# Performance work log

Measured on AMD Instinct MI355X. Metric: run time of the kernel, lower is better.

The kernel has to match this reference:

```python
import jax, jax.numpy as jnp
import numpy as np

N_NODES = 100000
N_EDGES = 1600000
D_IN = 128
D_OUT = 128


def setup_inputs() -> dict:
    key = jax.random.key(0)
    k1, k2, k3, k4 = jax.random.split(key, 4)
    feat = jax.random.normal(k1, (N_NODES, D_IN), dtype=jnp.float32)
    weight = jax.random.normal(k2, (D_IN, D_OUT), dtype=jnp.float32) * (1.0 / np.sqrt(D_IN))
    src = jax.random.randint(k3, (N_EDGES,), 0, N_NODES, dtype=jnp.int64)
    dst = jax.random.randint(k4, (N_EDGES,), 0, N_NODES, dtype=jnp.int64)
    return {"feat": feat, "weight": weight, "src": src, "dst": dst}


def reference(feat, weight, src, dst):
    n = feat.shape[0]
    ones = jnp.ones(src.shape[0], dtype=feat.dtype)
    # norm == 'both': scale source features by out_degree^{-1/2}
    out_deg = jnp.clip(jax.ops.segment_sum(ones, src, num_segments=n), 1.0)
    feat_src = feat * (out_deg ** -0.5)[:, None]  # [N, D_in]
    # update_all(copy_src, sum): gather src features, segment-sum into dst
    agg = jax.ops.segment_sum(feat_src[src], dst, num_segments=n)  # [N, D_in]
    # dense transform with external weight
    rst = agg @ weight  # [N, D_out]
    # destination-side normalization by in_degree^{-1/2}
    in_deg = jnp.clip(jax.ops.segment_sum(ones, dst, num_segments=n), 1.0)
    rst = rst * (in_deg ** -0.5)[:, None]
    return rst
```

## Files before the change

### kernel.cpp

```cpp
#include <hip/hip_runtime.h>
#include <stdint.h>


#define DIM 128
#define BK 64
#define MAXB 2048
#define CAPB 1280
#define SK 128
#define MAXS 1024
#define CAPS 2560
#define PT 512
#define EPT 13
#define CHUNK (PT * EPT)

typedef unsigned int uint;
typedef unsigned short ushortT;
typedef __attribute__((ext_vector_type(8))) _Float16 f16x8;
typedef __attribute__((ext_vector_type(4))) float f32x4;

__device__ __forceinline__ ushortT f2bf(float x) {
    uint u = __float_as_uint(x);
    u = (u + 0x7FFFu + ((u >> 16) & 1u)) >> 16;
    return (ushortT)u;
}
__device__ __forceinline__ float bflo(uint u) { return __uint_as_float(u << 16); }
__device__ __forceinline__ float bfhi(uint u) { return __uint_as_float(u & 0xffff0000u); }

union H16 { _Float16 h; ushortT u; };
__device__ __forceinline__ ushortT f2h_bits(float x) {
    H16 t; t.h = (_Float16)x; return t.u;
}

#define OFF_CD    0
#define OFF_LOFD  8192
#define OFF_CS    16384
#define OFF_LOFS  20480
#define OFF_BUFD  24576
#define OFF_BUFB  51200
#define OFF_BUFS  64512
#define OFF_WTOT  71168
#define SMEM_SZ   71232

__global__ __launch_bounds__(PT) void fusedA(
    const int* __restrict__ src, const int* __restrict__ dst,
    int* __restrict__ curB, int* __restrict__ curS,
    int* __restrict__ pairs, unsigned char* __restrict__ srcb,
    const float* __restrict__ feat, const float* __restrict__ W,
    ushortT* __restrict__ h,
    int E, int NPB, int NPS, int M, int NPART) {
    __shared__ __align__(16) unsigned char smem[SMEM_SZ];

    int bid = blockIdx.x;
    int tid = threadIdx.x;

    if (bid < NPART) {
        int* cD = (int*)(smem + OFF_CD);
        int* lofD = (int*)(smem + OFF_LOFD);
        int* cS = (int*)(smem + OFF_CS);
        int* lofS = (int*)(smem + OFF_LOFS);
        int* bufD = (int*)(smem + OFF_BUFD);
        ushortT* bufB = (ushortT*)(smem + OFF_BUFB);
        unsigned char* bufS = (unsigned char*)(smem + OFF_BUFS);
        int* wtotD = (int*)(smem + OFF_WTOT);
        int* wtotS = wtotD + 8;

        long long base = (long long)bid * CHUNK;
        for (int i = tid; i < MAXB; i += PT) cD[i] = 0;
        for (int i = tid; i < MAXS; i += PT) cS[i] = 0;
        __syncthreads();

        int sv[EPT], dv[EPT], lrD[EPT], lrS[EPT];
#pragma unroll
        for (int j = 0; j < EPT; ++j) {
            long long e = base + tid + j * PT;
            bool ok = e < E;
            int s = 0, d = 0;
            if (ok) { s = src[e]; d = dst[e]; }
            sv[j] = s; dv[j] = d;
            lrD[j] = ok ? atomicAdd(&cD[d >> 6], 1) : 0;
            lrS[j] = ok ? atomicAdd(&cS[s >> 7], 1) : 0;
        }
        __syncthreads();

        {
            int lane = tid & 63, wv = tid >> 6;
            int b0 = tid << 2;
            int s0 = cD[b0], s1 = cD[b0 + 1], s2 = cD[b0 + 2], s3 = cD[b0 + 3];
            int tsum = s0 + s1 + s2 + s3;
            int incl = tsum;
            for (int o = 1; o < 64; o <<= 1) {
                int y = __shfl_up(incl, o, 64);
                if (lane >= o) incl += y;
            }
            if (lane == 63) wtotD[wv] = incl;

            int a0idx = tid << 1;
            int t0 = cS[a0idx], t1 = cS[a0idx + 1];
            int ssum = t0 + t1;
            int sincl = ssum;
            for (int o = 1; o < 64; o <<= 1) {
                int y = __shfl_up(sincl, o, 64);
                if (lane >= o) sincl += y;
            }
            if (lane == 63) wtotS[wv] = sincl;
            __syncthreads();

            int wbD = 0, wbS = 0;
            for (int x = 0; x < wv; ++x) { wbD += wtotD[x]; wbS += wtotS[x]; }
            int exD = wbD + incl - tsum;
            lofD[b0] = exD;
            lofD[b0 + 1] = exD + s0;
            lofD[b0 + 2] = exD + s0 + s1;
            lofD[b0 + 3] = exD + s0 + s1 + s2;
            int exS = wbS + sincl - ssum;
            lofS[a0idx] = exS;
            lofS[a0idx + 1] = exS + t0;
        }
        __syncthreads();

        for (int i = tid; i < NPB; i += PT) {
            int c = cD[i];
            cD[i] = c ? atomicAdd(&curB[i], c) : 0;
        }
        for (int i = tid; i < NPS; i += PT) {
            int c = cS[i];
            cS[i] = c ? atomicAdd(&curS[i], c) : 0;
        }

#pragma unroll
        for (int j = 0; j < EPT; ++j) {
            long long e = base + tid + j * PT;
            if (e < E) {
                int b = dv[j] >> 6;
                int pos = lofD[b] + lrD[j];
                bufD[pos] = (sv[j] << 6) | (dv[j] & 63);
                bufB[pos] = (ushortT)b;
                bufS[lofS[sv[j] >> 7] + lrS[j]] = (unsigned char)(sv[j] & 127);
            }
        }
        __syncthreads();

        int cntE = (int)(((long long)E - base < (long long)CHUNK) ? (E - base) : CHUNK);
        for (int i = tid; i < cntE; i += PT) {
            int b = bufB[i];
            int pos = cD[b] + (i - lofD[b]);
            if (pos < CAPB) pairs[(size_t)b * CAPB + pos] = bufD[i];
        }
        for (int i = tid; i < cntE; i += PT) {
            int lo = 0, hi = NPS - 1;
            while (lo < hi) { int mid = (lo + hi + 1) >> 1; if (lofS[mid] <= i) lo = mid; else hi = mid - 1; }
            int pos = cS[lo] + (i - lofS[lo]);
            if (pos < CAPS) srcb[(size_t)lo * CAPS + pos] = bufS[i];
        }
    } else {
        ushortT* Bs = (ushortT*)smem;

        {
            int kk = (tid >> 3) << 1;
            int n0 = (tid & 7) << 4;
            const float* w0 = &W[(size_t)kk * DIM + n0];
            const float* w1 = w0 + DIM;
#pragma unroll
            for (int jj = 0; jj < 4; ++jj) {
                float4 a = *(const float4*)&w0[jj * 4];
                float4 b = *(const float4*)&w1[jj * 4];
                float av[4] = {a.x, a.y, a.z, a.w};
                float bv[4] = {b.x, b.y, b.z, b.w};
#pragma unroll
                for (int t = 0; t < 4; ++t) {
                    int n = n0 + jj * 4 + t;
                    uint u = (uint)f2h_bits(av[t]) | ((uint)f2h_bits(bv[t]) << 16);
                    int idx = n * 128 + (((kk >> 3) ^ (n & 7)) << 3) + (kk & 7);
                    *(uint*)&Bs[idx] = u;
                }
            }
        }
        __syncthreads();

        int wid = tid >> 6;
        int l = tid & 63;
        int lr = l & 15;
        int lk = l >> 4;
        int g = bid - NPART;
        int m0 = g * 128;
        int row = m0 + wid * 16 + lr;
        int rr = (row < M) ? row : 0;
        const float* fp = feat + (size_t)rr * DIM;

        f32x4 acc[8];
        f32x4 z = {0.f, 0.f, 0.f, 0.f};
#pragma unroll
        for (int n = 0; n < 8; ++n) acc[n] = z;

#pragma unroll
        for (int kc = 0; kc < 4; ++kc) {
            int kb = kc * 32 + lk * 8;
            float4 x0 = *(const float4*)&fp[kb];
            float4 x1 = *(const float4*)&fp[kb + 4];
            float f[8] = {x0.x, x0.y, x0.z, x0.w, x1.x, x1.y, x1.z, x1.w};
            f16x8 ah, al;
#pragma unroll
            for (int j = 0; j < 8; ++j) {
                _Float16 hi = (_Float16)f[j];
                ah[j] = hi;
                al[j] = (_Float16)(f[j] - (float)hi);
            }
#pragma unroll
            for (int n = 0; n < 8; ++n) {
                int brow = n * 16 + lr;
                int bidx = brow * 128 + (kb ^ ((brow & 7) << 3));
                f16x8 b = *(const f16x8*)&Bs[bidx];
                acc[n] = __builtin_amdgcn_mfma_f32_16x16x32_f16(ah, b, acc[n], 0, 0, 0);
                acc[n] = __builtin_amdgcn_mfma_f32_16x16x32_f16(al, b, acc[n], 0, 0, 0);
            }
        }

#pragma unroll
        for (int r = 0; r < 4; ++r) {
            int ro = m0 + wid * 16 + lk * 4 + r;
            if (ro < M) {
                uint w0 = (uint)f2bf(acc[0][r]) | ((uint)f2bf(acc[1][r]) << 16);
                uint w1 = (uint)f2bf(acc[2][r]) | ((uint)f2bf(acc[3][r]) << 16);
                uint w2 = (uint)f2bf(acc[4][r]) | ((uint)f2bf(acc[5][r]) << 16);
                uint w3 = (uint)f2bf(acc[6][r]) | ((uint)f2bf(acc[7][r]) << 16);
                uint4 o = make_uint4(w0, w1, w2, w3);
                *(uint4*)&h[(size_t)ro * DIM + (lr << 3)] = o;
            }
        }
    }
}

__global__ __launch_bounds__(256) void deg(
    const int* __restrict__ curS, const unsigned char* __restrict__ srcb,
    float* __restrict__ oscale, int N) {
    __shared__ int hist[SK];
    int p = blockIdx.x, tid = threadIdx.x;
    if (tid < SK) hist[tid] = 0;
    __syncthreads();
    int cnt = min(curS[p], CAPS);
    const unsigned char* b = &srcb[(size_t)p * CAPS];
    for (int i = tid; i < cnt; i += 256) atomicAdd(&hist[b[i]], 1);
    __syncthreads();
    if (tid < SK) {
        int node = p * SK + tid;
        if (node < N) oscale[node] = rsqrtf((float)max(hist[tid], 1));
    }
}

__global__ __launch_bounds__(512) void aggp(
    const ushortT* __restrict__ h, const int* __restrict__ pairs,
    const int* __restrict__ curB, const float* __restrict__ oscale,
    float* __restrict__ out, int N) {
    __shared__ int raw[CAPB];
    __shared__ int sorted[CAPB];
    __shared__ int hist[64], offs[64], cur[64];
    int p = blockIdx.x;
    int tid = threadIdx.x;
    if (tid < 64) hist[tid] = 0;
    __syncthreads();
    int cnt = min(curB[p], CAPB);
    const int* pb = &pairs[(size_t)p * CAPB];
    for (int i = tid; i < cnt; i += 512) {
        int w = pb[i];
        raw[i] = w;
        atomicAdd(&hist[w & 63], 1);
    }
    __syncthreads();
    if (tid < 64) {
        int x = hist[tid], incl = x;
        for (int o = 1; o < 64; o <<= 1) {
            int y = __shfl_up(incl, o, 64);
            if (tid >= o) incl += y;
        }
        offs[tid] = incl - x;
        cur[tid] = incl - x;
    }
    __syncthreads();
    for (int i = tid; i < cnt; i += 512) {
        int w = raw[i];
        int slot = atomicAdd(&cur[w & 63], 1);
        sorted[slot] = w >> 6;
    }
    __syncthreads();
    int g = tid >> 4, c = tid & 15;
    int cb = c << 3;
    for (int nd = g; nd < 64; nd += 32) {
        int node = p * BK + nd;
        if (node >= N) continue;
        int start = offs[nd];
        int degn = hist[nd];
        int end = min(start + degn, CAPB);
        float a0 = 0.f, a1 = 0.f, a2 = 0.f, a3 = 0.f;
        float a4 = 0.f, a5 = 0.f, a6 = 0.f, a7 = 0.f;
        int e = start;
        for (; e + 8 <= end; e += 8) {
            int s0 = sorted[e],     s1 = sorted[e + 1];
            int s2 = sorted[e + 2], s3 = sorted[e + 3];
            int s4 = sorted[e + 4], s5 = sorted[e + 5];
            int s6 = sorted[e + 6], s7 = sorted[e + 7];
            float o0 = oscale[s0], o1 = oscale[s1], o2 = oscale[s2], o3 = oscale[s3];
            float o4 = oscale[s4], o5 = oscale[s5], o6 = oscale[s6], o7 = oscale[s7];
            uint4 v0 = *(const uint4*)&h[(size_t)s0 * DIM + cb];
            uint4 v1 = *(const uint4*)&h[(size_t)s1 * DIM + cb];
            uint4 v2 = *(const uint4*)&h[(size_t)s2 * DIM + cb];
            uint4 v3 = *(const uint4*)&h[(size_t)s3 * DIM + cb];
            uint4 v4 = *(const uint4*)&h[(size_t)s4 * DIM + cb];
            uint4 v5 = *(const uint4*)&h[(size_t)s5 * DIM + cb];
            uint4 v6 = *(const uint4*)&h[(size_t)s6 * DIM + cb];
            uint4 v7 = *(const uint4*)&h[(size_t)s7 * DIM + cb];
            a0 += ((o0 * bflo(v0.x) + o1 * bflo(v1.x)) + (o2 * bflo(v2.x) + o3 * bflo(v3.x))) +
                  ((o4 * bflo(v4.x) + o5 * bflo(v5.x)) + (o6 * bflo(v6.x) + o7 * bflo(v7.x)));
            a1 += ((o0 * bfhi(v0.x) + o1 * bfhi(v1.x)) + (o2 * bfhi(v2.x) + o3 * bfhi(v3.x))) +
                  ((o4 * bfhi(v4.x) + o5 * bfhi(v5.x)) + (o6 * bfhi(v6.x) + o7 * bfhi(v7.x)));
            a2 += ((o0 * bflo(v0.y) + o1 * bflo(v1.y)) + (o2 * bflo(v2.y) + o3 * bflo(v3.y))) +
                  ((o4 * bflo(v4.y) + o5 * bflo(v5.y)) + (o6 * bflo(v6.y) + o7 * bflo(v7.y)));
            a3 += ((o0 * bfhi(v0.y) + o1 * bfhi(v1.y)) + (o2 * bfhi(v2.y) + o3 * bfhi(v3.y))) +
                  ((o4 * bfhi(v4.y) + o5 * bfhi(v5.y)) + (o6 * bfhi(v6.y) + o7 * bfhi(v7.y)));
            a4 += ((o0 * bflo(v0.z) + o1 * bflo(v1.z)) + (o2 * bflo(v2.z) + o3 * bflo(v3.z))) +
                  ((o4 * bflo(v4.z) + o5 * bflo(v5.z)) + (o6 * bflo(v6.z) + o7 * bflo(v7.z)));
            a5 += ((o0 * bfhi(v0.z) + o1 * bfhi(v1.z)) + (o2 * bfhi(v2.z) + o3 * bfhi(v3.z))) +
                  ((o4 * bfhi(v4.z) + o5 * bfhi(v5.z)) + (o6 * bfhi(v6.z) + o7 * bfhi(v7.z)));
            a6 += ((o0 * bflo(v0.w) + o1 * bflo(v1.w)) + (o2 * bflo(v2.w) + o3 * bflo(v3.w))) +
                  ((o4 * bflo(v4.w) + o5 * bflo(v5.w)) + (o6 * bflo(v6.w) + o7 * bflo(v7.w)));
            a7 += ((o0 * bfhi(v0.w) + o1 * bfhi(v1.w)) + (o2 * bfhi(v2.w) + o3 * bfhi(v3.w))) +
                  ((o4 * bfhi(v4.w) + o5 * bfhi(v5.w)) + (o6 * bfhi(v6.w) + o7 * bfhi(v7.w)));
        }
        for (; e < end; ++e) {
            int se = sorted[e];
            float os = oscale[se];
            uint4 v = *(const uint4*)&h[(size_t)se * DIM + cb];
            a0 += os * bflo(v.x); a1 += os * bfhi(v.x);
            a2 += os * bflo(v.y); a3 += os * bfhi(v.y);
            a4 += os * bflo(v.z); a5 += os * bfhi(v.z);
            a6 += os * bflo(v.w); a7 += os * bfhi(v.w);
        }
        float scn = rsqrtf((float)max(degn, 1));
        size_t ob = (size_t)node * DIM + c;
        out[ob]       = a0 * scn;
        out[ob + 16]  = a1 * scn;
        out[ob + 32]  = a2 * scn;
        out[ob + 48]  = a3 * scn;
        out[ob + 64]  = a4 * scn;
        out[ob + 80]  = a5 * scn;
        out[ob + 96]  = a6 * scn;
        out[ob + 112] = a7 * scn;
    }
}

extern "C" void kernel_launch(void* const* d_in, const int* in_sizes, int n_in,
                              void* d_out, int out_size, void* d_ws, size_t ws_size,
                              hipStream_t stream) {
    const float* feat = (const float*)d_in[0];
    const float* W    = (const float*)d_in[1];
    const int*   src  = (const int*)d_in[2];
    const int*   dst  = (const int*)d_in[3];
    float* out = (float*)d_out;

    int N = in_sizes[0] / DIM;
    int E = in_sizes[2];
    int NPB = (N + BK - 1) / BK;
    int NPS = (N + SK - 1) / SK;

    int* curB = (int*)d_ws;
    int* curS = curB + NPB;
    float* oscale = (float*)(curS + NPS);
    int* pairs = (int*)(oscale + N);
    unsigned char* srcb = (unsigned char*)(pairs + (size_t)NPB * CAPB);
    uintptr_t hp = (uintptr_t)(srcb + (size_t)NPS * CAPS);
    ushortT* h = (ushortT*)((hp + 15) & ~(uintptr_t)15);

    hipMemsetAsync(curB, 0, (size_t)(NPB + NPS) * sizeof(int), stream);

    int NPART = (E + CHUNK - 1) / CHUNK;
    int NGEMM = (N + 127) / 128;

    fusedA<<<NPART + NGEMM, PT, 0, stream>>>(src, dst, curB, curS, pairs, srcb,
                                             feat, W, h, E, NPB, NPS, N, NPART);
    deg<<<NPS, 256, 0, stream>>>(curS, srcb, oscale, N);
    aggp<<<NPB, 512, 0, stream>>>(h, pairs, curB, oscale, out, N);
}
```

Before: 226.6 us.

## Merge partition, GEMM, degree and aggregation into one cooperative persistent kernel

Replaces the memset plus three kernel launches with a single cooperative kernel that zeroes counters, partitions edges, runs GEMM tiles and the aggregation through atomic ticket work queues, and separates phases with grid-wide syncs. The aim is to remove launch and inter-kernel gaps and to balance load with persistent blocks. In exchange, the GEMM can no longer overlap with the partition phase, grid syncs add their own cost, and the grid is capped at two blocks per CU across 256 CUs.

Measured after the change: 337.3 us. +48.8%, slower.

```diff
diff --git a/kernel.cpp b/kernel.cpp
--- a/kernel.cpp
+++ b/kernel.cpp
@@ -1,5 +1,8 @@
 #include <hip/hip_runtime.h>
+#include <hip/hip_cooperative_groups.h>
 #include <stdint.h>
+
+namespace cg = cooperative_groups;
 
 
 #define DIM 128
@@ -41,19 +44,25 @@
 #define OFF_WTOT  71168
 #define SMEM_SZ   71232
 
-__global__ __launch_bounds__(PT) void fusedA(
+__global__ __launch_bounds__(PT) void mega(
     const int* __restrict__ src, const int* __restrict__ dst,
-    int* __restrict__ curB, int* __restrict__ curS,
+    int* __restrict__ curB, int* __restrict__ curS, int* __restrict__ ctrs,
     int* __restrict__ pairs, unsigned char* __restrict__ srcb,
     const float* __restrict__ feat, const float* __restrict__ W,
-    ushortT* __restrict__ h,
-    int E, int NPB, int NPS, int M, int NPART) {
+    ushortT* __restrict__ h, float* __restrict__ oscale,
+    float* __restrict__ out,
+    int E, int N, int NPB, int NPS, int NPART, int NGEMM) {
+    cg::grid_group gg = cg::this_grid();
     __shared__ __align__(16) unsigned char smem[SMEM_SZ];
-
-    int bid = blockIdx.x;
-    int tid = threadIdx.x;
-
-    if (bid < NPART) {
+    __shared__ int tkt;
+
+    int b = blockIdx.x, tid = threadIdx.x, GD = gridDim.x;
+
+    int ztot = NPB + NPS + 2;
+    for (int i = b * PT + tid; i < ztot; i += GD * PT) curB[i] = 0;
+    gg.sync();
+
+    for (int c = b; c < NPART; c += GD) {
         int* cD = (int*)(smem + OFF_CD);
         int* lofD = (int*)(smem + OFF_LOFD);
         int* cS = (int*)(smem + OFF_CS);
@@ -64,7 +73,7 @@
         int* wtotD = (int*)(smem + OFF_WTOT);
         int* wtotS = wtotD + 8;
 
-        long long base = (long long)bid * CHUNK;
+        long long base = (long long)c * CHUNK;
         for (int i = tid; i < MAXB; i += PT) cD[i] = 0;
         for (int i = tid; i < MAXS; i += PT) cS[i] = 0;
         __syncthreads();
@@ -119,22 +128,22 @@
         __syncthreads();
 
         for (int i = tid; i < NPB; i += PT) {
-            int c = cD[i];
-            cD[i] = c ? atomicAdd(&curB[i], c) : 0;
+            int cc = cD[i];
+            cD[i] = cc ? atomicAdd(&curB[i], cc) : 0;
         }
         for (int i = tid; i < NPS; i += PT) {
-            int c = cS[i];
-            cS[i] = c ? atomicAdd(&curS[i], c) : 0;
+            int cc = cS[i];
+            cS[i] = cc ? atomicAdd(&curS[i], cc) : 0;
         }
 
 #pragma unroll
         for (int j = 0; j < EPT; ++j) {
             long long e = base + tid + j * PT;
             if (e < E) {
-                int b = dv[j] >> 6;
-                int pos = lofD[b] + lrD[j];
+                int bb = dv[j] >> 6;
+                int pos = lofD[bb] + lrD[j];
                 bufD[pos] = (sv[j] << 6) | (dv[j] & 63);
-                bufB[pos] = (ushortT)b;
+                bufB[pos] = (ushortT)bb;
                 bufS[lofS[sv[j] >> 7] + lrS[j]] = (unsigned char)(sv[j] & 127);
             }
         }
@@ -142,9 +151,9 @@
 
         int cntE = (int)(((long long)E - base < (long long)CHUNK) ? (E - base) : CHUNK);
         for (int i = tid; i < cntE; i += PT) {
-            int b = bufB[i];
-            int pos = cD[b] + (i - lofD[b]);
-            if (pos < CAPB) pairs[(size_t)b * CAPB + pos] = bufD[i];
+            int bb = bufB[i];
+            int pos = cD[bb] + (i - lofD[bb]);
+            if (pos < CAPB) pairs[(size_t)bb * CAPB + pos] = bufD[i];
         }
         for (int i = tid; i < cntE; i += PT) {
             int lo = 0, hi = NPS - 1;
@@ -152,9 +161,17 @@
             int pos = cS[lo] + (i - lofS[lo]);
             if (pos < CAPS) srcb[(size_t)lo * CAPS + pos] = bufS[i];
         }
-    } else {
+        __syncthreads();
+    }
+
+    for (;;) {
+        __syncthreads();
+        if (tid == 0) tkt = atomicAdd(&ctrs[0], 1);
+        __syncthreads();
+        int t = tkt;
+        if (t >= NGEMM) break;
+
         ushortT* Bs = (ushortT*)smem;
-
         {
             int kk = (tid >> 3) << 1;
             int n0 = (tid & 7) << 4;
@@ -163,15 +180,15 @@
 #pragma unroll
             for (int jj = 0; jj < 4; ++jj) {
                 float4 a = *(const float4*)&w0[jj * 4];
-                float4 b = *(const float4*)&w1[jj * 4];
+                float4 bq = *(const float4*)&w1[jj * 4];
                 float av[4] = {a.x, a.y, a.z, a.w};
-                float bv[4] = {b.x, b.y, b.z, b.w};
-#pragma unroll
-                for (int t = 0; t < 4; ++t) {
-                    int n = n0 + jj * 4 + t;
-                    uint u = (uint)f2h_bits(av[t]) | ((uint)f2h_bits(bv[t]) << 16);
+                float bv[4] = {bq.x, bq.y, bq.z, bq.w};
+#pragma unroll
+                for (int u = 0; u < 4; ++u) {
+                    int n = n0 + jj * 4 + u;
+                    uint uu = (uint)f2h_bits(av[u]) | ((uint)f2h_bits(bv[u]) << 16);
                     int idx = n * 128 + (((kk >> 3) ^ (n & 7)) << 3) + (kk & 7);
-                    *(uint*)&Bs[idx] = u;
+                    *(uint*)&Bs[idx] = uu;
                 }
             }
         }
@@ -181,10 +198,9 @@
         int l = tid & 63;
         int lr = l & 15;
         int lk = l >> 4;
-        int g = bid - NPART;
-        int m0 = g * 128;
+        int m0 = t * 128;
         int row = m0 + wid * 16 + lr;
-        int rr = (row < M) ? row : 0;
+        int rr = (row < N) ? row : 0;
         const float* fp = feat + (size_t)rr * DIM;
 
         f32x4 acc[8];
@@ -209,16 +225,16 @@
             for (int n = 0; n < 8; ++n) {
                 int brow = n * 16 + lr;
                 int bidx = brow * 128 + (kb ^ ((brow & 7) << 3));
-                f16x8 b = *(const f16x8*)&Bs[bidx];
-                acc[n] = __builtin_amdgcn_mfma_f32_16x16x32_f16(ah, b, acc[n], 0, 0, 0);
-                acc[n] = __builtin_amdgcn_mfma_f32_16x16x32_f16(al, b, acc[n], 0, 0, 0);
+                f16x8 bb = *(const f16x8*)&Bs[bidx];
+                acc[n] = __builtin_amdgcn_mfma_f32_16x16x32_f16(ah, bb, acc[n], 0, 0, 0);
+                acc[n] = __builtin_amdgcn_mfma_f32_16x16x32_f16(al, bb, acc[n], 0, 0, 0);
             }
         }
 
 #pragma unroll
         for (int r = 0; r < 4; ++r) {
             int ro = m0 + wid * 16 + lk * 4 + r;
-            if (ro < M) {
+            if (ro < N) {
                 uint w0 = (uint)f2bf(acc[0][r]) | ((uint)f2bf(acc[1][r]) << 16);
                 uint w1 = (uint)f2bf(acc[2][r]) | ((uint)f2bf(acc[3][r]) << 16);
                 uint w2 = (uint)f2bf(acc[4][r]) | ((uint)f2bf(acc[5][r]) << 16);
@@ -228,154 +244,164 @@
             }
         }
     }
-}
-
-__global__ __launch_bounds__(256) void deg(
-    const int* __restrict__ curS, const unsigned char* __restrict__ srcb,
-    float* __restrict__ oscale, int N) {
-    __shared__ int hist[SK];
-    int p = blockIdx.x, tid = threadIdx.x;
-    if (tid < SK) hist[tid] = 0;
-    __syncthreads();
-    int cnt = min(curS[p], CAPS);
-    const unsigned char* b = &srcb[(size_t)p * CAPS];
-    for (int i = tid; i < cnt; i += 256) atomicAdd(&hist[b[i]], 1);
-    __syncthreads();
-    if (tid < SK) {
-        int node = p * SK + tid;
-        if (node < N) oscale[node] = rsqrtf((float)max(hist[tid], 1));
+    gg.sync();
+
+    for (int p = b; p < NPS; p += GD) {
+        int* hist = (int*)smem;
+        if (tid < SK) hist[tid] = 0;
+        __syncthreads();
+        int cnt = min(curS[p], CAPS);
+        const unsigned char* bb = &srcb[(size_t)p * CAPS];
+        for (int i = tid; i < cnt; i += PT) atomicAdd(&hist[bb[i]], 1);
+        __syncthreads();
+        if (tid < SK) {
+            int node = p * SK + tid;
+            if (node < N) oscale[node] = rsqrtf((float)max(hist[tid], 1));
+        }
+        __syncthreads();
     }
-}
-
-__global__ __launch_bounds__(512) void aggp(
-    const ushortT* __restrict__ h, const int* __restrict__ pairs,
-    const int* __restrict__ curB, const float* __restrict__ oscale,
-    float* __restrict__ out, int N) {
-    __shared__ int raw[CAPB];
-    __shared__ int sorted[CAPB];
-    __shared__ int hist[64], offs[64], cur[64];
-    int p = blockIdx.x;
-    int tid = threadIdx.x;
-    if (tid < 64) hist[tid] = 0;
-    __syncthreads();
-    int cnt = min(curB[p], CAPB);
-    const int* pb = &pairs[(size_t)p * CAPB];
-    for (int i = tid; i < cnt; i += 512) {
-        int w = pb[i];
-        raw[i] = w;
-        atomicAdd(&hist[w & 63], 1);
-    }
-    __syncthreads();
-    if (tid < 64) {
-        int x = hist[tid], incl = x;
-        for (int o = 1; o < 64; o <<= 1) {
-            int y = __shfl_up(incl, o, 64);
-            if (tid >= o) incl += y;
-        }
-        offs[tid] = incl - x;
-        cur[tid] = incl - x;
-    }
-    __syncthreads();
-    for (int i = tid; i < cnt; i += 512) {
-        int w = raw[i];
-        int slot = atomicAdd(&cur[w & 63], 1);
-        sorted[slot] = w >> 6;
-    }
-    __syncthreads();
-    int g = tid >> 4, c = tid & 15;
-    int cb = c << 3;
-    for (int nd = g; nd < 64; nd += 32) {
-        int node = p * BK + nd;
-        if (node >= N) continue;
-        int start = offs[nd];
-        int degn = hist[nd];
-        int end = min(start + degn, CAPB);
-        float a0 = 0.f, a1 = 0.f, a2 = 0.f, a3 = 0.f;
-        float a4 = 0.f, a5 = 0.f, a6 = 0.f, a7 = 0.f;
-        int e = start;
-        for (; e + 8 <= end; e += 8) {
-            int s0 = sorted[e],     s1 = sorted[e + 1];
-            int s2 = sorted[e + 2], s3 = sorted[e + 3];
-            int s4 = sorted[e + 4], s5 = sorted[e + 5];
-            int s6 = sorted[e + 6], s7 = sorted[e + 7];
-            float o0 = oscale[s0], o1 = oscale[s1], o2 = oscale[s2], o3 = oscale[s3];
-            float o4 = oscale[s4], o5 = oscale[s5], o6 = oscale[s6], o7 = oscale[s7];
-            uint4 v0 = *(const uint4*)&h[(size_t)s0 * DIM + cb];
-            uint4 v1 = *(const uint4*)&h[(size_t)s1 * DIM + cb];
-            uint4 v2 = *(const uint4*)&h[(size_t)s2 * DIM + cb];
-            uint4 v3 = *(const uint4*)&h[(size_t)s3 * DIM + cb];
-            uint4 v4 = *(const uint4*)&h[(size_t)s4 * DIM + cb];
-            uint4 v5 = *(const uint4*)&h[(size_t)s5 * DIM + cb];
-            uint4 v6 = *(const uint4*)&h[(size_t)s6 * DIM + cb];
-            uint4 v7 = *(const uint4*)&h[(size_t)s7 * DIM + cb];
-            a0 += ((o0 * bflo(v0.x) + o1 * bflo(v1.x)) + (o2 * bflo(v2.x) + o3 * bflo(v3.x))) +
-                  ((o4 * bflo(v4.x) + o5 * bflo(v5.x)) + (o6 * bflo(v6.x) + o7 * bflo(v7.x)));
-            a1 += ((o0 * bfhi(v0.x) + o1 * bfhi(v1.x)) + (o2 * bfhi(v2.x) + o3 * bfhi(v3.x))) +
-                  ((o4 * bfhi(v4.x) + o5 * bfhi(v5.x)) + (o6 * bfhi(v6.x) + o7 * bfhi(v7.x)));
-            a2 += ((o0 * bflo(v0.y) + o1 * bflo(v1.y)) + (o2 * bflo(v2.y) + o3 * bflo(v3.y))) +
-                  ((o4 * bflo(v4.y) + o5 * bflo(v5.y)) + (o6 * bflo(v6.y) + o7 * bflo(v7.y)));
-            a3 += ((o0 * bfhi(v0.y) + o1 * bfhi(v1.y)) + (o2 * bfhi(v2.y) + o3 * bfhi(v3.y))) +
-                  ((o4 * bfhi(v4.y) + o5 * bfhi(v5.y)) + (o6 * bfhi(v6.y) + o7 * bfhi(v7.y)));
-            a4 += ((o0 * bflo(v0.z) + o1 * bflo(v1.z)) + (o2 * bflo(v2.z) + o3 * bflo(v3.z))) +
-                  ((o4 * bflo(v4.z) + o5 * bflo(v5.z)) + (o6 * bflo(v6.z) + o7 * bflo(v7.z)));
-            a5 += ((o0 * bfhi(v0.z) + o1 * bfhi(v1.z)) + (o2 * bfhi(v2.z) + o3 * bfhi(v3.z))) +
-                  ((o4 * bfhi(v4.z) + o5 * bfhi(v5.z)) + (o6 * bfhi(v6.z) + o7 * bfhi(v7.z)));
-            a6 += ((o0 * bflo(v0.w) + o1 * bflo(v1.w)) + (o2 * bflo(v2.w) + o3 * bflo(v3.w))) +
-                  ((o4 * bflo(v4.w) + o5 * bflo(v5.w)) + (o6 * bflo(v6.w) + o7 * bflo(v7.w)));
-            a7 += ((o0 * bfhi(v0.w) + o1 * bfhi(v1.w)) + (o2 * bfhi(v2.w) + o3 * bfhi(v3.w))) +
-                  ((o4 * bfhi(v4.w) + o5 * bfhi(v5.w)) + (o6 * bfhi(v6.w) + o7 * bfhi(v7.w)));
-        }
-        for (; e < end; ++e) {
-            int se = sorted[e];
-            float os = oscale[se];
-            uint4 v = *(const uint4*)&h[(size_t)se * DIM + cb];
-            a0 += os * bflo(v.x); a1 += os * bfhi(v.x);
-            a2 += os * bflo(v.y); a3 += os * bfhi(v.y);
-            a4 += os * bflo(v.z); a5 += os * bfhi(v.z);
-            a6 += os * bflo(v.w); a7 += os * bfhi(v.w);
-        }
-        float scn = rsqrtf((float)max(degn, 1));
-        size_t ob = (size_t)node * DIM + c;
-        out[ob]       = a0 * scn;
-        out[ob + 16]  = a1 * scn;
-        out[ob + 32]  = a2 * scn;
-        out[ob + 48]  = a3 * scn;
-        out[ob + 64]  = a4 * scn;
-        out[ob + 80]  = a5 * scn;
-        out[ob + 96]  = a6 * scn;
-        out[ob + 112] = a7 * scn;
+    gg.sync();
+
+    for (;;) {
+        __syncthreads();
+        if (tid == 0) tkt = atomicAdd(&ctrs[1], 1);
+        __syncthreads();
+        int p = tkt;
+        if (p >= NPB) break;
+
+        int* raw = (int*)smem;
+        int* sorted = (int*)(smem + 5120);
+        int* hist = (int*)(smem + 10240);
+        int* offs = (int*)(smem + 10496);
+        int* cur = (int*)(smem + 10752);
+
+        if (tid < 64) hist[tid] = 0;
+        __syncthreads();
+        int cnt = min(curB[p], CAPB);
+        const int* pb = &pairs[(size_t)p * CAPB];
+        for (int i = tid; i < cnt; i += PT) {
+            int w = pb[i];
+            raw[i] = w;
+            atomicAdd(&hist[w & 63], 1);
+        }
+        __syncthreads();
+        if (tid < 64) {
+            int x = hist[tid], incl = x;
+            for (int o = 1; o < 64; o <<= 1) {
+                int y = __shfl_up(incl, o, 64);
+                if (tid >= o) incl += y;
+            }
+            offs[tid] = incl - x;
+            cur[tid] = incl - x;
+        }
+        __syncthreads();
+        for (int i = tid; i < cnt; i += PT) {
+            int w = raw[i];
+            int slot = atomicAdd(&cur[w & 63], 1);
+            sorted[slot] = w >> 6;
+        }
+        __syncthreads();
+        int g = tid >> 4, c = tid & 15;
+        int cb = c << 3;
+        for (int nd = g; nd < 64; nd += 32) {
+            int node = p * BK + nd;
+            if (node >= N) continue;
+            int start = offs[nd];
+            int degn = hist[nd];
+            int end = min(start + degn, CAPB);
+            float a0 = 0.f, a1 = 0.f, a2 = 0.f, a3 = 0.f;
+            float a4 = 0.f, a5 = 0.f, a6 = 0.f, a7 = 0.f;
+            int e = start;
+            for (; e + 8 <= end; e += 8) {
+                int s0 = sorted[e],     s1 = sorted[e + 1];
+                int s2 = sorted[e + 2], s3 = sorted[e + 3];
+                int s4 = sorted[e + 4], s5 = sorted[e + 5];
+                int s6 = sorted[e + 6], s7 = sorted[e + 7];
+                float o0 = oscale[s0], o1 = oscale[s1], o2 = oscale[s2], o3 = oscale[s3];
+                float o4 = oscale[s4], o5 = oscale[s5], o6 = oscale[s6], o7 = oscale[s7];
+                uint4 v0 = *(const uint4*)&h[(size_t)s0 * DIM + cb];
+                uint4 v1 = *(const uint4*)&h[(size_t)s1 * DIM + cb];
+                uint4 v2 = *(const uint4*)&h[(size_t)s2 * DIM + cb];
+                uint4 v3 = *(const uint4*)&h[(size_t)s3 * DIM + cb];
+                uint4 v4 = *(const uint4*)&h[(size_t)s4 * DIM + cb];
+                uint4 v5 = *(const uint4*)&h[(size_t)s5 * DIM + cb];
+                uint4 v6 = *(const uint4*)&h[(size_t)s6 * DIM + cb];
+                uint4 v7 = *(const uint4*)&h[(size_t)s7 * DIM + cb];
+                a0 += ((o0 * bflo(v0.x) + o1 * bflo(v1.x)) + (o2 * bflo(v2.x) + o3 * bflo(v3.x))) +
+                      ((o4 * bflo(v4.x) + o5 * bflo(v5.x)) + (o6 * bflo(v6.x) + o7 * bflo(v7.x)));
+                a1 += ((o0 * bfhi(v0.x) + o1 * bfhi(v1.x)) + (o2 * bfhi(v2.x) + o3 * bfhi(v3.x))) +
+                      ((o4 * bfhi(v4.x) + o5 * bfhi(v5.x)) + (o6 * bfhi(v6.x) + o7 * bfhi(v7.x)));
+                a2 += ((o0 * bflo(v0.y) + o1 * bflo(v1.y)) + (o2 * bflo(v2.y) + o3 * bflo(v3.y))) +
+                      ((o4 * bflo(v4.y) + o5 * bflo(v5.y)) + (o6 * bflo(v6.y) + o7 * bflo(v7.y)));
+                a3 += ((o0 * bfhi(v0.y) + o1 * bfhi(v1.y)) + (o2 * bfhi(v2.y) + o3 * bfhi(v3.y))) +
+                      ((o4 * bfhi(v4.y) + o5 * bfhi(v5.y)) + (o6 * bfhi(v6.y) + o7 * bfhi(v7.y)));
+                a4 += ((o0 * bflo(v0.z) + o1 * bflo(v1.z)) + (o2 * bflo(v2.z) + o3 * bflo(v3.z))) +
+                      ((o4 * bflo(v4.z) + o5 * bflo(v5.z)) + (o6 * bflo(v6.z) + o7 * bflo(v7.z)));
+                a5 += ((o0 * bfhi(v0.z) + o1 * bfhi(v1.z)) + (o2 * bfhi(v2.z) + o3 * bfhi(v3.z))) +
+                      ((o4 * bfhi(v4.z) + o5 * bfhi(v5.z)) + (o6 * bfhi(v6.z) + o7 * bfhi(v7.z)));
+                a6 += ((o0 * bflo(v0.w) + o1 * bflo(v1.w)) + (o2 * bflo(v2.w) + o3 * bflo(v3.w))) +
+                      ((o4 * bflo(v4.w) + o5 * bflo(v5.w)) + (o6 * bflo(v6.w) + o7 * bflo(v7.w)));
+                a7 += ((o0 * bfhi(v0.w) + o1 * bfhi(v1.w)) + (o2 * bfhi(v2.w) + o3 * bfhi(v3.w))) +
+                      ((o4 * bfhi(v4.w) + o5 * bfhi(v5.w)) + (o6 * bfhi(v6.w) + o7 * bfhi(v7.w)));
+            }
+            for (; e < end; ++e) {
+                int se = sorted[e];
+                float os = oscale[se];
+                uint4 v = *(const uint4*)&h[(size_t)se * DIM + cb];
+                a0 += os * bflo(v.x); a1 += os * bfhi(v.x);
+                a2 += os * bflo(v.y); a3 += os * bfhi(v.y);
+                a4 += os * bflo(v.z); a5 += os * bfhi(v.z);
+                a6 += os * bflo(v.w); a7 += os * bfhi(v.w);
+            }
+            float scn = rsqrtf((float)max(degn, 1));
+            size_t ob = (size_t)node * DIM + c;
+            out[ob]       = a0 * scn;
+            out[ob + 16]  = a1 * scn;
+            out[ob + 32]  = a2 * scn;
+            out[ob + 48]  = a3 * scn;
+            out[ob + 64]  = a4 * scn;
+            out[ob + 80]  = a5 * scn;
+            out[ob + 96]  = a6 * scn;
+            out[ob + 112] = a7 * scn;
+        }
     }
 }
 
 extern "C" void kernel_launch(void* const* d_in, const int* in_sizes, int n_in,
                               void* d_out, int out_size, void* d_ws, size_t ws_size,
                               hipStream_t stream) {
+    const int* src  = (const int*)d_in[2];
+    const int* dst  = (const int*)d_in[3];
     const float* feat = (const float*)d_in[0];
     const float* W    = (const float*)d_in[1];
-    const int*   src  = (const int*)d_in[2];
-    const int*   dst  = (const int*)d_in[3];
     float* out = (float*)d_out;
 
     int N = in_sizes[0] / DIM;
     int E = in_sizes[2];
     int NPB = (N + BK - 1) / BK;
     int NPS = (N + SK - 1) / SK;
+    int NPART = (E + CHUNK - 1) / CHUNK;
+    int NGEMM = (N + 127) / 128;
 
     int* curB = (int*)d_ws;
     int* curS = curB + NPB;
-    float* oscale = (float*)(curS + NPS);
+    int* ctrs = curS + NPS;
+    float* oscale = (float*)(ctrs + 2);
     int* pairs = (int*)(oscale + N);
     unsigned char* srcb = (unsigned char*)(pairs + (size_t)NPB * CAPB);
     uintptr_t hp = (uintptr_t)(srcb + (size_t)NPS * CAPS);
     ushortT* h = (ushortT*)((hp + 15) & ~(uintptr_t)15);
 
-    hipMemsetAsync(curB, 0, (size_t)(NPB + NPS) * sizeof(int), stream);
-
-    int NPART = (E + CHUNK - 1) / CHUNK;
-    int NGEMM = (N + 127) / 128;
-
-    fusedA<<<NPART + NGEMM, PT, 0, stream>>>(src, dst, curB, curS, pairs, srcb,
-                                             feat, W, h, E, NPB, NPS, N, NPART);
-    deg<<<NPS, 256, 0, stream>>>(curS, srcb, oscale, N);
-    aggp<<<NPB, 512, 0, stream>>>(h, pairs, curB, oscale, out, N);
+    int bpc = 0;
+    hipOccupancyMaxActiveBlocksPerMultiprocessor(&bpc, mega, PT, 0);
+    if (bpc < 1) bpc = 1;
+    if (bpc > 2) bpc = 2;
+    int grid = bpc * 256;
+
+    void* args[] = {
+        (void*)&src, (void*)&dst, (void*)&curB, (void*)&curS, (void*)&ctrs,
+        (void*)&pairs, (void*)&srcb, (void*)&feat, (void*)&W, (void*)&h,
+        (void*)&oscale, (void*)&out,
+        (void*)&E, (void*)&N, (void*)&NPB, (void*)&NPS, (void*)&NPART, (void*)&NGEMM};
+    hipLaunchCooperativeKernel((void*)mega, dim3(grid), dim3(PT), args, 0, stream);
 }
```
